# Optimization experiments

Hardware: AMD Instinct MI355X
Metric: run time of the kernel (lower is better)

Reference implementation:

```python
import jax, jax.numpy as jnp
import numpy as np

K = 7        # kernel_size
STRIDE = 1
PAD = 3
DIL = 1


def setup_inputs() -> dict:
    key = jax.random.key(0)
    k1, k2 = jax.random.split(key)
    # input: [N, C, H, W]; weight: [N, C_w, k*k, H_out, W_out], C_w = C // share_planes
    input_ = jax.random.normal(k1, (16, 256, 32, 32), dtype=jnp.float32)
    weight = jax.random.uniform(k2, (16, 32, K * K, 32, 32), dtype=jnp.float32)
    return {"input_": input_, "weight": weight}


def reference(input_, weight):
    n, c_x, H, W = input_.shape
    c_w = weight.shape[1]  # shared channels; share_planes = c_x // c_w
    # Unfold: patches has channels ordered channel-major (c * k*k + kk),
    # matching torch.nn.Unfold's layout. Shape: [n, c_x*K*K, out_h, out_w]
    patches = jax.lax.conv_general_dilated_patches(
        input_,
        filter_shape=(K, K),
        window_strides=(STRIDE, STRIDE),
        padding=[(PAD, PAD), (PAD, PAD)],
        rhs_dilation=(DIL, DIL),
        dimension_numbers=("NCHW", "OIHW", "NCHW"),
    )
    out_h, out_w = patches.shape[2], patches.shape[3]
    # [n, groups, c_w, k*k, out_h, out_w]
    patches = patches.reshape(n, c_x // c_w, c_w, K * K, out_h, out_w)
    # weight: [n, c_w, k*k, out_h, out_w] broadcast over groups; sum over kernel dim
    out = jnp.einsum("ngckhw,nckhw->ngchw", patches, weight)
    return out.reshape(n, c_x, out_h, out_w)
```

## Files before the change

kernel.cpp:

```cpp
#include <hip/hip_runtime.h>


#define KS   7
#define PAD  3
#define HH   32
#define WW   32
#define CW   32
#define GG   8
#define CX   256
#define PROW 38
#define PSTR 40

__global__ __launch_bounds__(256, 2)
void aggregation_kernel(const float* __restrict__ input,
                        const float* __restrict__ weight,
                        float* __restrict__ out) {
    __shared__ float lds[GG * PROW * PSTR];

    const int t  = threadIdx.x;
    const int cc = blockIdx.x & (CW - 1);
    const int n  = blockIdx.x >> 5;

    float4* lz = reinterpret_cast<float4*>(lds);
    #pragma unroll
    for (int i = 0; i < 12; ++i) {
        int idx = t + i * 256;
        if (idx < GG * PROW * PSTR / 4)
            lz[idx] = make_float4(0.f, 0.f, 0.f, 0.f);
    }
    __syncthreads();

    const float* inbase = input + (size_t)n * CX * HH * WW;
    #pragma unroll
    for (int j = 0; j < 8; ++j) {
        int idx = t + j * 256;
        int ch  = idx >> 8;
        int rem = idx & 255;
        int r   = rem >> 3;
        int c4  = (rem & 7) << 2;
        float4 v = *reinterpret_cast<const float4*>(
            inbase + ((size_t)(ch * CW + cc) * HH + r) * WW + c4);
        float* dst = &lds[(ch * PROW + (r + PAD)) * PSTR + (c4 + PAD)];
        dst[0] = v.x; dst[1] = v.y; dst[2] = v.z; dst[3] = v.w;
    }
    __syncthreads();

    const int h  = t >> 3;
    const int w0 = (t & 7) << 2;

    float acc[GG][4];
    #pragma unroll
    for (int g = 0; g < GG; ++g)
        #pragma unroll
        for (int p = 0; p < 4; ++p) acc[g][p] = 0.f;

    const float* wbase = weight
        + ((size_t)n * CW + cc) * (KS * KS) * (HH * WW)
        + h * WW + w0;

    float4 wv[KS], wn[KS];

    #pragma unroll
    for (int kw = 0; kw < KS; ++kw)
        wv[kw] = *reinterpret_cast<const float4*>(wbase + (size_t)kw * (HH * WW));

    auto compute_row = [&](int kh, const float4 (&wrow)[KS]) {
        const int row = h + kh;
        #pragma unroll
        for (int g = 0; g < GG; ++g) {
            const float4* rp = reinterpret_cast<const float4*>(
                &lds[(g * PROW + row) * PSTR + w0]);
            float4 r0 = rp[0], r1 = rp[1], r2 = rp[2];
            float rr[12] = {r0.x, r0.y, r0.z, r0.w,
                            r1.x, r1.y, r1.z, r1.w,
                            r2.x, r2.y, r2.z, r2.w};
            #pragma unroll
            for (int kw = 0; kw < KS; ++kw) {
                acc[g][0] = fmaf(rr[kw + 0], wrow[kw].x, acc[g][0]);
                acc[g][1] = fmaf(rr[kw + 1], wrow[kw].y, acc[g][1]);
                acc[g][2] = fmaf(rr[kw + 2], wrow[kw].z, acc[g][2]);
                acc[g][3] = fmaf(rr[kw + 3], wrow[kw].w, acc[g][3]);
            }
        }
    };

    for (int kh = 0; kh < KS - 1; ++kh) {
        #pragma unroll
        for (int kw = 0; kw < KS; ++kw)
            wn[kw] = *reinterpret_cast<const float4*>(
                wbase + (size_t)((kh + 1) * KS + kw) * (HH * WW));
        compute_row(kh, wv);
        #pragma unroll
        for (int kw = 0; kw < KS; ++kw) wv[kw] = wn[kw];
    }
    compute_row(KS - 1, wv);

    #pragma unroll
    for (int g = 0; g < GG; ++g) {
        float4 o = make_float4(acc[g][0], acc[g][1], acc[g][2], acc[g][3]);
        *reinterpret_cast<float4*>(
            out + (((size_t)n * CX + g * CW + cc) * HH + h) * WW + w0) = o;
    }
}

extern "C" void kernel_launch(void* const* d_in, const int* in_sizes, int n_in,
                              void* d_out, int out_size, void* d_ws, size_t ws_size,
                              hipStream_t stream) {
    const float* input  = (const float*)d_in[0];
    const float* weight = (const float*)d_in[1];
    float* out = (float*)d_out;
    aggregation_kernel<<<dim3(16 * CW), dim3(256), 0, stream>>>(input, weight, out);
}
```

Measured before the change: 168.5 us.

## Split rows and channel groups across more blocks to raise occupancy

Each block now handles half the output rows, and its threads split the 8 channel groups into two halves of 4. This doubles the grid size and cuts per-thread accumulators, and launch bounds allow 4 blocks per CU. The aim is more latency hiding on the memory-bound weight stream. In exchange, each weight element is loaded twice per block (once per group half), and the explicit software prefetch of the next weight row is removed.

Measured after the change: 169.0 us. Within noise of the previous version (+0.3%).

```diff
diff --git a/kernel.cpp b/kernel.cpp
--- a/kernel.cpp
+++ b/kernel.cpp
@@ -7,23 +7,28 @@
 #define WW   32
 #define CW   32
 #define GG   8
+#define GH   4
 #define CX   256
-#define PROW 38
+#define HB   16
+#define PROW (HB + 2*PAD)
 #define PSTR 40
 
-__global__ __launch_bounds__(256, 2)
+__global__ __launch_bounds__(256, 4)
 void aggregation_kernel(const float* __restrict__ input,
                         const float* __restrict__ weight,
                         float* __restrict__ out) {
     __shared__ float lds[GG * PROW * PSTR];
 
-    const int t  = threadIdx.x;
-    const int cc = blockIdx.x & (CW - 1);
-    const int n  = blockIdx.x >> 5;
+    const int t   = threadIdx.x;
+    const int bid = blockIdx.x;
+    const int hs  = bid & 1;
+    const int cc  = (bid >> 1) & (CW-1);
+    const int n   = bid >> 6;
+    const int h0  = hs * HB;
 
     float4* lz = reinterpret_cast<float4*>(lds);
     #pragma unroll
-    for (int i = 0; i < 12; ++i) {
+    for (int i = 0; i < 7; ++i) {
         int idx = t + i * 256;
         if (idx < GG * PROW * PSTR / 4)
             lz[idx] = make_float4(0.f, 0.f, 0.f, 0.f);
@@ -32,42 +37,51 @@
 
     const float* inbase = input + (size_t)n * CX * HH * WW;
     #pragma unroll
-    for (int j = 0; j < 8; ++j) {
+    for (int j = 0; j < 6; ++j) {
         int idx = t + j * 256;
-        int ch  = idx >> 8;
-        int rem = idx & 255;
-        int r   = rem >> 3;
-        int c4  = (rem & 7) << 2;
-        float4 v = *reinterpret_cast<const float4*>(
-            inbase + ((size_t)(ch * CW + cc) * HH + r) * WW + c4);
-        float* dst = &lds[(ch * PROW + (r + PAD)) * PSTR + (c4 + PAD)];
-        dst[0] = v.x; dst[1] = v.y; dst[2] = v.z; dst[3] = v.w;
+        if (idx < GG * PROW * 8) {
+            int ch  = idx / (PROW * 8);
+            int rem = idx - ch * (PROW * 8);
+            int r   = rem >> 3;
+            int q   = rem & 7;
+            int gr  = h0 - PAD + r;
+            if (gr >= 0 && gr < HH) {
+                float4 v = *reinterpret_cast<const float4*>(
+                    inbase + ((size_t)(ch * CW + cc) * HH + gr) * WW + (q << 2));
+                float* dst = &lds[(ch * PROW + r) * PSTR + (q << 2) + PAD];
+                dst[0] = v.x; dst[1] = v.y; dst[2] = v.z; dst[3] = v.w;
+            }
+        }
     }
     __syncthreads();
 
-    const int h  = t >> 3;
-    const int w0 = (t & 7) << 2;
+    const int gh  = t >> 7;
+    const int pos = t & 127;
+    const int hr  = pos >> 3;
+    const int w0  = (pos & 7) << 2;
+    const int h   = h0 + hr;
 
-    float acc[GG][4];
+    float acc[GH][4];
     #pragma unroll
-    for (int g = 0; g < GG; ++g)
+    for (int gi = 0; gi < GH; ++gi)
         #pragma unroll
-        for (int p = 0; p < 4; ++p) acc[g][p] = 0.f;
+        for (int p = 0; p < 4; ++p) acc[gi][p] = 0.f;
 
     const float* wbase = weight
         + ((size_t)n * CW + cc) * (KS * KS) * (HH * WW)
         + h * WW + w0;
 
-    float4 wv[KS], wn[KS];
-
     #pragma unroll
-    for (int kw = 0; kw < KS; ++kw)
-        wv[kw] = *reinterpret_cast<const float4*>(wbase + (size_t)kw * (HH * WW));
-
-    auto compute_row = [&](int kh, const float4 (&wrow)[KS]) {
-        const int row = h + kh;
+    for (int kh = 0; kh < KS; ++kh) {
+        float4 wv[KS];
         #pragma unroll
-        for (int g = 0; g < GG; ++g) {
+        for (int kw = 0; kw < KS; ++kw)
+            wv[kw] = *reinterpret_cast<const float4*>(
+                wbase + (size_t)(kh * KS + kw) * (HH * WW));
+        const int row = hr + kh;
+        #pragma unroll
+        for (int gi = 0; gi < GH; ++gi) {
+            const int g = gh * GH + gi;
             const float4* rp = reinterpret_cast<const float4*>(
                 &lds[(g * PROW + row) * PSTR + w0]);
             float4 r0 = rp[0], r1 = rp[1], r2 = rp[2];
@@ -76,28 +90,18 @@
                             r2.x, r2.y, r2.z, r2.w};
             #pragma unroll
             for (int kw = 0; kw < KS; ++kw) {
-                acc[g][0] = fmaf(rr[kw + 0], wrow[kw].x, acc[g][0]);
-                acc[g][1] = fmaf(rr[kw + 1], wrow[kw].y, acc[g][1]);
-                acc[g][2] = fmaf(rr[kw + 2], wrow[kw].z, acc[g][2]);
-                acc[g][3] = fmaf(rr[kw + 3], wrow[kw].w, acc[g][3]);
+                acc[gi][0] = fmaf(rr[kw + 0], wv[kw].x, acc[gi][0]);
+                acc[gi][1] = fmaf(rr[kw + 1], wv[kw].y, acc[gi][1]);
+                acc[gi][2] = fmaf(rr[kw + 2], wv[kw].z, acc[gi][2]);
+                acc[gi][3] = fmaf(rr[kw + 3], wv[kw].w, acc[gi][3]);
             }
         }
-    };
-
-    for (int kh = 0; kh < KS - 1; ++kh) {
-        #pragma unroll
-        for (int kw = 0; kw < KS; ++kw)
-            wn[kw] = *reinterpret_cast<const float4*>(
-                wbase + (size_t)((kh + 1) * KS + kw) * (HH * WW));
-        compute_row(kh, wv);
-        #pragma unroll
-        for (int kw = 0; kw < KS; ++kw) wv[kw] = wn[kw];
     }
-    compute_row(KS - 1, wv);
 
     #pragma unroll
-    for (int g = 0; g < GG; ++g) {
-        float4 o = make_float4(acc[g][0], acc[g][1], acc[g][2], acc[g][3]);
+    for (int gi = 0; gi < GH; ++gi) {
+        const int g = gh * GH + gi;
+        float4 o = make_float4(acc[gi][0], acc[gi][1], acc[gi][2], acc[gi][3]);
         *reinterpret_cast<float4*>(
             out + (((size_t)n * CX + g * CW + cc) * HH + h) * WW + w0) = o;
     }
@@ -109,5 +113,5 @@
     const float* input  = (const float*)d_in[0];
     const float* weight = (const float*)d_in[1];
     float* out = (float*)d_out;
-    aggregation_kernel<<<dim3(16 * CW), dim3(256), 0, stream>>>(input, weight, out);
+    aggregation_kernel<<<dim3(16 * CW * 2), dim3(256), 0, stream>>>(input, weight, out);
 }
```
